# Kernel optimization log

Hardware: AMD Instinct MI355X
Metric: run time of the kernel (lower is better)

The kernel has to match this reference:

```python
import jax, jax.numpy as jnp
import numpy as np

N_NODES = 10000


def _sage_conv(x, src, dst, W_l, W_r, b):
    # mean aggregation of source features at destination nodes (PyG SAGEConv default)
    msg = x[src]                                             # [E, C_in]
    agg = jax.ops.segment_sum(msg, dst, num_segments=N_NODES)  # [N, C_in]
    cnt = jax.ops.segment_sum(jnp.ones((src.shape[0],), x.dtype), dst,
                              num_segments=N_NODES)
    mean = agg / jnp.maximum(cnt, 1.0)[:, None]              # isolated nodes -> 0
    return mean @ W_l + x @ W_r + b


def setup_inputs() -> dict:
    key = jax.random.key(0)
    ks = jax.random.split(key, 8)
    E = 640000
    x = jax.random.normal(ks[0], (N_NODES, 128), dtype=jnp.float32)
    edge_index = jax.random.randint(ks[1], (2, E), 0, N_NODES, dtype=jnp.int64)
    W1_l = jax.random.normal(ks[2], (128, 256), dtype=jnp.float32) * 0.05
    W1_r = jax.random.normal(ks[3], (128, 256), dtype=jnp.float32) * 0.05
    b1 = jnp.zeros((256,), dtype=jnp.float32)
    W2_l = jax.random.normal(ks[4], (256, 128), dtype=jnp.float32) * 0.05
    W2_r = jax.random.normal(ks[5], (256, 128), dtype=jnp.float32) * 0.05
    b2 = jnp.zeros((128,), dtype=jnp.float32)
    return {"x": x, "edge_index": edge_index, "W1_l": W1_l, "W1_r": W1_r,
            "b1": b1, "W2_l": W2_l, "W2_r": W2_r, "b2": b2}


def reference(x, edge_index, W1_l, W1_r, b1, W2_l, W2_r, b2):
    src, dst = edge_index[0], edge_index[1]
    h = jax.nn.relu(_sage_conv(x, src, dst, W1_l, W1_r, b1))
    out = _sage_conv(h, src, dst, W2_l, W2_r, b2)
    return out
```

## Files before the change

kernel.cpp:

```cpp
#include <hip/hip_runtime.h>

#define N_NODES 10000
#define HB 128

typedef unsigned int uint;
typedef unsigned short ushort;
typedef __attribute__((ext_vector_type(8))) short bf16x8;
typedef __attribute__((ext_vector_type(4))) float f32x4;

__device__ __forceinline__ ushort f2bf(float f) {
    uint b = __float_as_uint(f);
    b += 0x7fffu + ((b >> 16) & 1u);
    return (ushort)(b >> 16);
}

#define CAST_B 1250
#define TCAST_B 512

__global__ __launch_bounds__(256) void prep_kernel(const float* __restrict__ x,
                                                   const float* __restrict__ W1l,
                                                   const float* __restrict__ W1r,
                                                   const float* __restrict__ W2l,
                                                   const float* __restrict__ W2r,
                                                   const int* __restrict__ dst, int E, int chunk,
                                                   int* __restrict__ chunk_hist,
                                                   ushort* __restrict__ lrank,
                                                   ushort* __restrict__ xb,
                                                   ushort* __restrict__ W1T,
                                                   ushort* __restrict__ W2T,
                                                   int* __restrict__ aggv) {
    __shared__ int hist[N_NODES];
    int b = blockIdx.x;
    int t = threadIdx.x;
    if (b < HB) {
        int4* h4 = (int4*)hist;
        for (int i = t; i < N_NODES / 4; i += 256) h4[i] = make_int4(0, 0, 0, 0);
        __syncthreads();
        int e0 = b * chunk;
        int e1 = e0 + chunk; if (e1 > E) e1 = E;
        for (int e = e0 + t; e < e1; e += 256) {
            int d = dst[e];
            lrank[e] = (ushort)atomicAdd(&hist[d], 1);
        }
        __syncthreads();
        int4* c4 = (int4*)(chunk_hist + b * N_NODES);
        for (int i = t; i < N_NODES / 4; i += 256) c4[i] = h4[i];
    } else if (b < HB + CAST_B) {
        if (b == HB && t < 64) aggv[t] = 0;
        int i = (b - HB) * 256 + t;
        float4 v = ((const float4*)x)[i];
        ushort4 o;
        o.x = f2bf(v.x); o.y = f2bf(v.y); o.z = f2bf(v.z); o.w = f2bf(v.w);
        ((ushort4*)xb)[i] = o;
    } else {
        int id = (b - HB - CAST_B) * 256 + t;
        int z = id >> 16;
        int k = (id >> 8) & 255;
        int c = id & 255;
        if (z == 0) {
            float v = (k < 128) ? W1l[k * 256 + c] : W1r[(k - 128) * 256 + c];
            W1T[c * 256 + k] = f2bf(v);
        } else {
            float v = (c < 128) ? W2l[k * 128 + c] : W2r[k * 128 + (c - 128)];
            W2T[c * 256 + k] = f2bf(v);
        }
    }
}

__global__ __launch_bounds__(256) void csr_mid_kernel(int* __restrict__ ch,
                                                      int* __restrict__ row_ptr,
                                                      int* __restrict__ aggv) {
    int b = blockIdx.x, t = threadIdx.x;
    int n = b * 256 + t;
    bool ok = n < N_NODES;
    int s = 0;
    if (ok) {
#pragma unroll 8
        for (int c = 0; c < HB; ++c) s += ch[c * N_NODES + n];
    }
    int lane = t & 63, wid = t >> 6;
    int incl = s;
#pragma unroll
    for (int off = 1; off < 64; off <<= 1) {
        int y = __shfl_up(incl, off);
        if (lane >= off) incl += y;
    }
    __shared__ int wsum[4];
    __shared__ int sbase;
    if (lane == 63) wsum[wid] = incl;
    __syncthreads();
    int tot = wsum[0] + wsum[1] + wsum[2] + wsum[3];
    int wbase = 0;
#pragma unroll
    for (int w = 0; w < 4; ++w)
        if (w < wid) wbase += wsum[w];
    incl += wbase;
    if (t == 0)
        __hip_atomic_store(&aggv[b], tot + 1, __ATOMIC_RELEASE, __HIP_MEMORY_SCOPE_AGENT);
    if (t < 64) {
        int v = 0;
        if (t < b) {
            do {
                v = __hip_atomic_load(&aggv[t], __ATOMIC_ACQUIRE, __HIP_MEMORY_SCOPE_AGENT);
            } while (v == 0);
            --v;
        }
#pragma unroll
        for (int m = 1; m < 64; m <<= 1) v += __shfl_xor(v, m);
        if (t == 0) sbase = v;
    }
    __syncthreads();
    int base = sbase;
    if (b == 0 && t == 0) row_ptr[0] = 0;
    if (ok) {
        row_ptr[n + 1] = base + incl;
        int run = base + incl - s;
#pragma unroll 8
        for (int c = 0; c < HB; ++c) {
            int v = ch[c * N_NODES + n];
            ch[c * N_NODES + n] = run;
            run += v;
        }
    }
}

__global__ __launch_bounds__(256) void scatter_kernel(const int* __restrict__ src,
                                                      const int* __restrict__ dst,
                                                      const ushort* __restrict__ lrank,
                                                      const int* __restrict__ off,
                                                      int E, int chunk,
                                                      ushort* __restrict__ csr) {
    int g = blockIdx.x * blockDim.x + threadIdx.x;
    int e = g * 4;
    if (e + 3 < E) {
        int b = e / chunk;
        const int* ob = off + b * N_NODES;
        int4 d = *(const int4*)&dst[e];
        int4 s = *(const int4*)&src[e];
        ushort4 r = *(const ushort4*)&lrank[e];
        csr[ob[d.x] + r.x] = (ushort)s.x;
        csr[ob[d.y] + r.y] = (ushort)s.y;
        csr[ob[d.z] + r.z] = (ushort)s.z;
        csr[ob[d.w] + r.w] = (ushort)s.w;
    } else {
        for (; e < E; ++e)
            csr[off[(e / chunk) * N_NODES + dst[e]] + lrank[e]] = (ushort)src[e];
    }
}

template <int MODE>
__global__ __launch_bounds__(256) void agg_kernel(const ushort* __restrict__ feat,
                                                  const int* __restrict__ row_ptr,
                                                  const ushort* __restrict__ csr,
                                                  uint* __restrict__ outb,
                                                  float* __restrict__ out) {
    int wave = threadIdx.x >> 6;
    int lane = threadIdx.x & 63;
    int n = blockIdx.x * 4 + wave;
    if (n >= N_NODES) return;
    int beg = row_ptr[n], end = row_ptr[n + 1];
    const uint* f = (const uint*)feat;
    float ax0 = 0, ay0 = 0, ax1 = 0, ay1 = 0, ax2 = 0, ay2 = 0, ax3 = 0, ay3 = 0;
    int i = beg;
    for (; i + 8 <= end; i += 8) {
        int s0 = csr[i + 0];
        int s1 = csr[i + 1];
        int s2 = csr[i + 2];
        int s3 = csr[i + 3];
        int s4 = csr[i + 4];
        int s5 = csr[i + 5];
        int s6 = csr[i + 6];
        int s7 = csr[i + 7];
        uint u0 = f[s0 * 64 + lane];
        uint u1 = f[s1 * 64 + lane];
        uint u2 = f[s2 * 64 + lane];
        uint u3 = f[s3 * 64 + lane];
        uint u4 = f[s4 * 64 + lane];
        uint u5 = f[s5 * 64 + lane];
        uint u6 = f[s6 * 64 + lane];
        uint u7 = f[s7 * 64 + lane];
        ax0 += __uint_as_float(u0 << 16); ay0 += __uint_as_float(u0 & 0xffff0000u);
        ax1 += __uint_as_float(u1 << 16); ay1 += __uint_as_float(u1 & 0xffff0000u);
        ax2 += __uint_as_float(u2 << 16); ay2 += __uint_as_float(u2 & 0xffff0000u);
        ax3 += __uint_as_float(u3 << 16); ay3 += __uint_as_float(u3 & 0xffff0000u);
        ax0 += __uint_as_float(u4 << 16); ay0 += __uint_as_float(u4 & 0xffff0000u);
        ax1 += __uint_as_float(u5 << 16); ay1 += __uint_as_float(u5 & 0xffff0000u);
        ax2 += __uint_as_float(u6 << 16); ay2 += __uint_as_float(u6 & 0xffff0000u);
        ax3 += __uint_as_float(u7 << 16); ay3 += __uint_as_float(u7 & 0xffff0000u);
    }
    for (; i + 4 <= end; i += 4) {
        int s0 = csr[i + 0];
        int s1 = csr[i + 1];
        int s2 = csr[i + 2];
        int s3 = csr[i + 3];
        uint u0 = f[s0 * 64 + lane];
        uint u1 = f[s1 * 64 + lane];
        uint u2 = f[s2 * 64 + lane];
        uint u3 = f[s3 * 64 + lane];
        ax0 += __uint_as_float(u0 << 16); ay0 += __uint_as_float(u0 & 0xffff0000u);
        ax1 += __uint_as_float(u1 << 16); ay1 += __uint_as_float(u1 & 0xffff0000u);
        ax2 += __uint_as_float(u2 << 16); ay2 += __uint_as_float(u2 & 0xffff0000u);
        ax3 += __uint_as_float(u3 << 16); ay3 += __uint_as_float(u3 & 0xffff0000u);
    }
    for (; i < end; ++i) {
        int s = csr[i];
        uint u = f[s * 64 + lane];
        ax0 += __uint_as_float(u << 16); ay0 += __uint_as_float(u & 0xffff0000u);
    }
    float deg = (float)(end - beg);
    float inv = deg > 0.f ? 1.0f / deg : 0.0f;
    float sx = ((ax0 + ax1) + (ax2 + ax3)) * inv;
    float sy = ((ay0 + ay1) + (ay2 + ay3)) * inv;
    if (MODE == 0) {
        outb[n * 64 + lane] = (uint)f2bf(sx) | ((uint)f2bf(sy) << 16);
    } else {
        float2* o = (float2*)&out[n * 128 + lane * 2];
        float2 prev = *o;
        prev.x += sx; prev.y += sy;
        *o = prev;
    }
}

__global__ __launch_bounds__(256) void gemm_fused(const ushort* __restrict__ m1b,
                                                  const ushort* __restrict__ xb,
                                                  const ushort* __restrict__ W1T,
                                                  const float* __restrict__ b1,
                                                  const ushort* __restrict__ W2T,
                                                  const float* __restrict__ b2,
                                                  ushort* __restrict__ t,
                                                  float* __restrict__ out) {
    __shared__ ushort hsh[16 * 264];
    int w = threadIdx.x >> 6, lane = threadIdx.x & 63;
    int lr = lane & 15, lg = lane >> 4;
    int r0 = blockIdx.x * 16;
    int row = r0 + lr;
    int c0 = w * 64;

    bf16x8 afr[8];
#pragma unroll
    for (int ks = 0; ks < 8; ++ks) {
        int k0 = ks * 32;
        const ushort* Ab = (k0 < 128) ? (m1b + row * 128 + k0) : (xb + row * 128 + (k0 - 128));
        afr[ks] = *(const bf16x8*)(Ab + lg * 8);
    }

    {
        f32x4 acc[4] = {};
#pragma unroll
        for (int ks = 0; ks < 8; ++ks) {
            int k0 = ks * 32;
#pragma unroll
            for (int cg = 0; cg < 4; ++cg) {
                int col = c0 + cg * 16 + lr;
                bf16x8 b = *(const bf16x8*)(W1T + col * 256 + k0 + lg * 8);
                acc[cg] = __builtin_amdgcn_mfma_f32_16x16x32_bf16(afr[ks], b, acc[cg], 0, 0, 0);
            }
        }
#pragma unroll
        for (int cg = 0; cg < 4; ++cg) {
            int col = c0 + cg * 16 + lr;
            float bias = b1[col];
#pragma unroll
            for (int i = 0; i < 4; ++i) {
                float v = acc[cg][i] + bias;
                v = v > 0.f ? v : 0.f;
                hsh[(lg * 4 + i) * 264 + col] = f2bf(v);
            }
        }
    }
    __syncthreads();

    bf16x8 afr2[8];
#pragma unroll
    for (int ks = 0; ks < 8; ++ks)
        afr2[ks] = *(const bf16x8*)&hsh[lr * 264 + ks * 32 + lg * 8];

    {
        f32x4 acc[4] = {};
#pragma unroll
        for (int ks = 0; ks < 8; ++ks) {
            int k0 = ks * 32;
#pragma unroll
            for (int cg = 0; cg < 4; ++cg) {
                int col = c0 + cg * 16 + lr;
                bf16x8 b = *(const bf16x8*)(W2T + col * 256 + k0 + lg * 8);
                acc[cg] = __builtin_amdgcn_mfma_f32_16x16x32_bf16(afr2[ks], b, acc[cg], 0, 0, 0);
            }
        }
#pragma unroll
        for (int cg = 0; cg < 4; ++cg) {
            int col = c0 + cg * 16 + lr;
            if (col < 128) {
#pragma unroll
                for (int i = 0; i < 4; ++i)
                    t[(r0 + lg * 4 + i) * 128 + col] = f2bf(acc[cg][i]);
            } else {
                int oc = col - 128;
                float bias = b2[oc];
#pragma unroll
                for (int i = 0; i < 4; ++i)
                    out[(r0 + lg * 4 + i) * 128 + oc] = acc[cg][i] + bias;
            }
        }
    }
}


extern "C" void kernel_launch(void* const* d_in, const int* in_sizes, int n_in,
                              void* d_out, int out_size, void* d_ws, size_t ws_size,
                              hipStream_t stream) {
    const float* x   = (const float*)d_in[0];
    const int* edge  = (const int*)d_in[1];
    const float* W1l = (const float*)d_in[2];
    const float* W1r = (const float*)d_in[3];
    const float* b1  = (const float*)d_in[4];
    const float* W2l = (const float*)d_in[5];
    const float* W2r = (const float*)d_in[6];
    const float* b2  = (const float*)d_in[7];
    float* out = (float*)d_out;

    int E = in_sizes[1] / 2;
    const int* src = edge;
    const int* dst = edge + E;
    int chunk = (((E + HB - 1) / HB) + 3) & ~3;

    ushort* m1b  = (ushort*)d_ws;
    ushort* hb   = m1b + (size_t)N_NODES * 128;
    ushort* xb   = hb + (size_t)N_NODES * 256;
    ushort* W1T  = xb + (size_t)N_NODES * 128;
    ushort* W2T  = W1T + 256 * 256;
    ushort* csr  = W2T + 256 * 256;
    ushort* lrank= csr + E;
    int* chist   = (int*)(lrank + E);
    int* row_ptr = chist + HB * N_NODES;
    int* aggv    = row_ptr + (N_NODES + 1);
    ushort* tb   = m1b;

    prep_kernel<<<HB + CAST_B + TCAST_B, 256, 0, stream>>>(x, W1l, W1r, W2l, W2r,
                                                           dst, E, chunk, chist, lrank,
                                                           xb, W1T, W2T, aggv);

    csr_mid_kernel<<<(N_NODES + 255) / 256, 256, 0, stream>>>(chist, row_ptr, aggv);

    scatter_kernel<<<(E / 4 + 255) / 256, 256, 0, stream>>>(src, dst, lrank, chist, E, chunk, csr);

    agg_kernel<0><<<(N_NODES + 3) / 4, 256, 0, stream>>>(xb, row_ptr, csr, (uint*)m1b, nullptr);

    gemm_fused<<<N_NODES / 16, 256, 0, stream>>>(m1b, xb, W1T, b1, W2T, b2, tb, out);

    agg_kernel<1><<<(N_NODES + 3) / 4, 256, 0, stream>>>(tb, row_ptr, csr, nullptr, out);
}
```

Measured before the change: 99.38 us.

## Fuse CSR prefix-scan into prep kernel via flag sync; vectorize CSR index loads

Result: slower. 119.6 us (+20.4%).

```diff
diff --git a/kernel.cpp b/kernel.cpp
--- a/kernel.cpp
+++ b/kernel.cpp
@@ -2,6 +2,7 @@
 
 #define N_NODES 10000
 #define HB 128
+#define NMID 40
 
 typedef unsigned int uint;
 typedef unsigned short ushort;
@@ -28,7 +29,9 @@
                                                    ushort* __restrict__ xb,
                                                    ushort* __restrict__ W1T,
                                                    ushort* __restrict__ W2T,
-                                                   int* __restrict__ aggv) {
+                                                   int* __restrict__ row_ptr,
+                                                   int* __restrict__ aggv,
+                                                   int* __restrict__ histdone) {
     __shared__ int hist[N_NODES];
     int b = blockIdx.x;
     int t = threadIdx.x;
@@ -45,14 +48,16 @@
         __syncthreads();
         int4* c4 = (int4*)(chunk_hist + b * N_NODES);
         for (int i = t; i < N_NODES / 4; i += 256) c4[i] = h4[i];
+        __syncthreads();
+        if (t == 0)
+            __hip_atomic_store(&histdone[b], 1, __ATOMIC_RELEASE, __HIP_MEMORY_SCOPE_AGENT);
     } else if (b < HB + CAST_B) {
-        if (b == HB && t < 64) aggv[t] = 0;
         int i = (b - HB) * 256 + t;
         float4 v = ((const float4*)x)[i];
         ushort4 o;
         o.x = f2bf(v.x); o.y = f2bf(v.y); o.z = f2bf(v.z); o.w = f2bf(v.w);
         ((ushort4*)xb)[i] = o;
-    } else {
+    } else if (b < HB + CAST_B + TCAST_B) {
         int id = (b - HB - CAST_B) * 256 + t;
         int z = id >> 16;
         int k = (id >> 8) & 255;
@@ -64,62 +69,64 @@
             float v = (c < 128) ? W2l[k * 128 + c] : W2r[k * 128 + (c - 128)];
             W2T[c * 256 + k] = f2bf(v);
         }
-    }
-}
-
-__global__ __launch_bounds__(256) void csr_mid_kernel(int* __restrict__ ch,
-                                                      int* __restrict__ row_ptr,
-                                                      int* __restrict__ aggv) {
-    int b = blockIdx.x, t = threadIdx.x;
-    int n = b * 256 + t;
-    bool ok = n < N_NODES;
-    int s = 0;
-    if (ok) {
+    } else {
+        int mb = b - (HB + CAST_B + TCAST_B);
+        if (t < HB) {
+            while (__hip_atomic_load(&histdone[t], __ATOMIC_ACQUIRE,
+                                     __HIP_MEMORY_SCOPE_AGENT) == 0)
+                __builtin_amdgcn_s_sleep(8);
+        }
+        __syncthreads();
+        __builtin_amdgcn_fence(__ATOMIC_ACQUIRE, "agent");
+
+        int n = mb * 256 + t;
+        bool ok = n < N_NODES;
+        int s = 0;
+        if (ok) {
 #pragma unroll 8
-        for (int c = 0; c < HB; ++c) s += ch[c * N_NODES + n];
-    }
-    int lane = t & 63, wid = t >> 6;
-    int incl = s;
-#pragma unroll
-    for (int off = 1; off < 64; off <<= 1) {
-        int y = __shfl_up(incl, off);
-        if (lane >= off) incl += y;
-    }
-    __shared__ int wsum[4];
-    __shared__ int sbase;
-    if (lane == 63) wsum[wid] = incl;
-    __syncthreads();
-    int tot = wsum[0] + wsum[1] + wsum[2] + wsum[3];
-    int wbase = 0;
-#pragma unroll
-    for (int w = 0; w < 4; ++w)
-        if (w < wid) wbase += wsum[w];
-    incl += wbase;
-    if (t == 0)
-        __hip_atomic_store(&aggv[b], tot + 1, __ATOMIC_RELEASE, __HIP_MEMORY_SCOPE_AGENT);
-    if (t < 64) {
-        int v = 0;
-        if (t < b) {
-            do {
-                v = __hip_atomic_load(&aggv[t], __ATOMIC_ACQUIRE, __HIP_MEMORY_SCOPE_AGENT);
-            } while (v == 0);
-            --v;
-        }
-#pragma unroll
-        for (int m = 1; m < 64; m <<= 1) v += __shfl_xor(v, m);
-        if (t == 0) sbase = v;
-    }
-    __syncthreads();
-    int base = sbase;
-    if (b == 0 && t == 0) row_ptr[0] = 0;
-    if (ok) {
-        row_ptr[n + 1] = base + incl;
-        int run = base + incl - s;
+            for (int c = 0; c < HB; ++c) s += chunk_hist[c * N_NODES + n];
+        }
+        int lane = t & 63, wid = t >> 6;
+        int incl = s;
+#pragma unroll
+        for (int off = 1; off < 64; off <<= 1) {
+            int y = __shfl_up(incl, off);
+            if (lane >= off) incl += y;
+        }
+        if (lane == 63) hist[wid] = incl;
+        __syncthreads();
+        int tot = hist[0] + hist[1] + hist[2] + hist[3];
+        int wbase = 0;
+#pragma unroll
+        for (int w = 0; w < 4; ++w)
+            if (w < wid) wbase += hist[w];
+        incl += wbase;
+        if (t == 0)
+            __hip_atomic_store(&aggv[mb], tot + 1, __ATOMIC_RELEASE, __HIP_MEMORY_SCOPE_AGENT);
+        if (t < 64) {
+            int v = 0;
+            if (t < mb) {
+                do {
+                    v = __hip_atomic_load(&aggv[t], __ATOMIC_ACQUIRE, __HIP_MEMORY_SCOPE_AGENT);
+                } while (v == 0);
+                --v;
+            }
+#pragma unroll
+            for (int m = 1; m < 64; m <<= 1) v += __shfl_xor(v, m);
+            if (t == 0) hist[4] = v;
+        }
+        __syncthreads();
+        int base = hist[4];
+        if (mb == 0 && t == 0) row_ptr[0] = 0;
+        if (ok) {
+            row_ptr[n + 1] = base + incl;
+            int run = base + incl - s;
 #pragma unroll 8
-        for (int c = 0; c < HB; ++c) {
-            int v = ch[c * N_NODES + n];
-            ch[c * N_NODES + n] = run;
-            run += v;
+            for (int c = 0; c < HB; ++c) {
+                int v = chunk_hist[c * N_NODES + n];
+                chunk_hist[c * N_NODES + n] = run;
+                run += v;
+            }
         }
     }
 }
@@ -162,15 +169,17 @@
     const uint* f = (const uint*)feat;
     float ax0 = 0, ay0 = 0, ax1 = 0, ay1 = 0, ax2 = 0, ay2 = 0, ax3 = 0, ay3 = 0;
     int i = beg;
+    for (; i < end && (i & 7); ++i) {
+        int s = csr[i];
+        uint u = f[s * 64 + lane];
+        ax0 += __uint_as_float(u << 16); ay0 += __uint_as_float(u & 0xffff0000u);
+    }
     for (; i + 8 <= end; i += 8) {
-        int s0 = csr[i + 0];
-        int s1 = csr[i + 1];
-        int s2 = csr[i + 2];
-        int s3 = csr[i + 3];
-        int s4 = csr[i + 4];
-        int s5 = csr[i + 5];
-        int s6 = csr[i + 6];
-        int s7 = csr[i + 7];
+        int4 cs = *(const int4*)&csr[i];
+        int s0 = cs.x & 0xffff, s1 = (int)((uint)cs.x >> 16);
+        int s2 = cs.y & 0xffff, s3 = (int)((uint)cs.y >> 16);
+        int s4 = cs.z & 0xffff, s5 = (int)((uint)cs.z >> 16);
+        int s6 = cs.w & 0xffff, s7 = (int)((uint)cs.w >> 16);
         uint u0 = f[s0 * 64 + lane];
         uint u1 = f[s1 * 64 + lane];
         uint u2 = f[s2 * 64 + lane];
@@ -188,20 +197,6 @@
         ax2 += __uint_as_float(u6 << 16); ay2 += __uint_as_float(u6 & 0xffff0000u);
         ax3 += __uint_as_float(u7 << 16); ay3 += __uint_as_float(u7 & 0xffff0000u);
     }
-    for (; i + 4 <= end; i += 4) {
-        int s0 = csr[i + 0];
-        int s1 = csr[i + 1];
-        int s2 = csr[i + 2];
-        int s3 = csr[i + 3];
-        uint u0 = f[s0 * 64 + lane];
-        uint u1 = f[s1 * 64 + lane];
-        uint u2 = f[s2 * 64 + lane];
-        uint u3 = f[s3 * 64 + lane];
-        ax0 += __uint_as_float(u0 << 16); ay0 += __uint_as_float(u0 & 0xffff0000u);
-        ax1 += __uint_as_float(u1 << 16); ay1 += __uint_as_float(u1 & 0xffff0000u);
-        ax2 += __uint_as_float(u2 << 16); ay2 += __uint_as_float(u2 & 0xffff0000u);
-        ax3 += __uint_as_float(u3 << 16); ay3 += __uint_as_float(u3 & 0xffff0000u);
-    }
     for (; i < end; ++i) {
         int s = csr[i];
         uint u = f[s * 64 + lane];
@@ -334,13 +329,14 @@
     int* chist   = (int*)(lrank + E);
     int* row_ptr = chist + HB * N_NODES;
     int* aggv    = row_ptr + (N_NODES + 1);
+    int* histdone= aggv + 64;
     ushort* tb   = m1b;
 
-    prep_kernel<<<HB + CAST_B + TCAST_B, 256, 0, stream>>>(x, W1l, W1r, W2l, W2r,
-                                                           dst, E, chunk, chist, lrank,
-                                                           xb, W1T, W2T, aggv);
-
-    csr_mid_kernel<<<(N_NODES + 255) / 256, 256, 0, stream>>>(chist, row_ptr, aggv);
+    hipMemsetAsync(aggv, 0, (64 + HB) * sizeof(int), stream);
+
+    prep_kernel<<<HB + CAST_B + TCAST_B + NMID, 256, 0, stream>>>(
+        x, W1l, W1r, W2l, W2r, dst, E, chunk, chist, lrank,
+        xb, W1T, W2T, row_ptr, aggv, histdone);
 
     scatter_kernel<<<(E / 4 + 255) / 256, 256, 0, stream>>>(src, dst, lrank, chist, E, chunk, csr);
 
```
